# Kernel optimization log

Measured on AMD Instinct MI355X. Metric: run time of the kernel, lower is better.

## Reference

```python
import jax, jax.numpy as jnp
import numpy as np

E = 8        # num_experts
K = 2        # num_experts_per_tok
H = 1024     # hidden_dim
F = 2816     # intermediate_dim
R = 256      # shared-core rank
B, S = 2, 1024


def setup_inputs() -> dict:
    key = jax.random.key(0)
    ks = jax.random.split(key, 12)
    inp = {
        "hidden_states": jax.random.normal(ks[0], (B, S, H), jnp.float32),
        "gate_w": jax.random.normal(ks[1], (H, E), jnp.float32) / np.sqrt(H),
        # gate_proj: hidden -> intermediate, factored W_e = Ug[e] @ Cg @ Vg[e]
        "Ug": jax.random.normal(ks[2], (E, H, R), jnp.float32) / np.sqrt(H),
        "Cg": jax.random.normal(ks[3], (R, R), jnp.float32) / np.sqrt(R),
        "Vg": jax.random.normal(ks[4], (E, R, F), jnp.float32) / np.sqrt(R),
        # up_proj: hidden -> intermediate
        "Uu": jax.random.normal(ks[5], (E, H, R), jnp.float32) / np.sqrt(H),
        "Cu": jax.random.normal(ks[6], (R, R), jnp.float32) / np.sqrt(R),
        "Vu": jax.random.normal(ks[7], (E, R, F), jnp.float32) / np.sqrt(R),
        # down_proj: intermediate -> hidden
        "Ud": jax.random.normal(ks[8], (E, F, R), jnp.float32) / np.sqrt(F),
        "Cd": jax.random.normal(ks[9], (R, R), jnp.float32) / np.sqrt(R),
        "Vd": jax.random.normal(ks[10], (E, R, H), jnp.float32) / np.sqrt(R),
    }
    return inp


def _moe_forward(x, gate_w, Ug, Cg, Vg, Uu, Cu, Vu, Ud, Cd, Vd):
    b, s, h = x.shape
    xf = x.reshape(-1, h)                       # [T, H]
    T = xf.shape[0]
    logits = xf @ gate_w                        # [T, E]
    probs = jax.nn.softmax(logits, axis=-1)
    w, idx = jax.lax.top_k(probs, K)            # [T, K]
    w = w / jnp.sum(w, axis=-1, keepdims=True)
    # dense combine weights: combine[t, e] = sum of renormalized routing
    # weights over top-k slots routed to expert e (scatter-add in torch code)
    combine = jnp.zeros((T, E), xf.dtype).at[jnp.arange(T)[:, None], idx].add(w)
    out = jnp.zeros_like(xf)
    for e in range(E):  # fixed small expert count
        g = (xf @ Ug[e]) @ Cg @ Vg[e]           # [T, F]
        u = (xf @ Uu[e]) @ Cu @ Vu[e]           # [T, F]
        a = jax.nn.silu(g) * u
        y = (a @ Ud[e]) @ Cd @ Vd[e]            # [T, H]
        out = out + combine[:, e:e + 1] * y
    return out.reshape(b, s, h)


def reference(hidden_states, gate_w, Ug, Cg, Vg, Uu, Cu, Vu, Ud, Cd, Vd):
    return _moe_forward(hidden_states, gate_w, Ug, Cg, Vg, Uu, Cu, Vu, Ud, Cd, Vd)
```

## Files before the change

### kernel.cpp

```cpp
#include <hip/hip_runtime.h>
#include <math.h>

constexpr int cE = 8;
constexpr int cH = 1024;
constexpr int cF = 2816;
constexpr int cR = 256;
constexpr int cT = 2048;
constexpr int ROWS = cT * 2;
constexpr int LDA = 40;

using short8  = __attribute__((ext_vector_type(8))) short;
using float4v = __attribute__((ext_vector_type(4))) float;
#define MFMA16 __builtin_amdgcn_mfma_f32_16x16x32_bf16

__device__ __forceinline__ unsigned short f2bf(float f) {
  union { float f; unsigned u; } v; v.f = f;
  unsigned r = v.u + 0x7fffu + ((v.u >> 16) & 1u);
  return (unsigned short)(r >> 16);
}
__device__ __forceinline__ float bf2f(unsigned short s) {
  union { unsigned u; float f; } v; v.u = (unsigned)s << 16; return v.f;
}

__device__ __forceinline__ void store_bf8(unsigned short* dst, float4 a, float4 b) {
  union { unsigned short u[8]; uint4 v; } t;
  t.u[0] = f2bf(a.x); t.u[1] = f2bf(a.y); t.u[2] = f2bf(a.z); t.u[3] = f2bf(a.w);
  t.u[4] = f2bf(b.x); t.u[5] = f2bf(b.y); t.u[6] = f2bf(b.z); t.u[7] = f2bf(b.w);
  *reinterpret_cast<uint4*>(dst) = t.v;
}

__device__ __forceinline__ void gld16(const unsigned short* g, unsigned short* l) {
  __builtin_amdgcn_global_load_lds(
      (const __attribute__((address_space(1))) void*)g,
      (__attribute__((address_space(3))) void*)l, 16, 0, 0);
}

__device__ __forceinline__ void tconv_tile64(
    const float* __restrict__ in, unsigned short* __restrict__ out,
    int P, int Q, int e, int bx, int by, int tid, float (*tile)[65])
{
  const long es = (long)P * Q;
  in += e * es; out += e * es;
  const int c0 = bx * 64, r0 = by * 64;
  const int r = tid >> 4, c4 = (tid & 15) * 4;
#pragma unroll
  for (int p = 0; p < 4; ++p) {
    float4 v = *reinterpret_cast<const float4*>(
        in + (long)(r0 + p * 16 + r) * Q + c0 + c4);
    tile[p * 16 + r][c4 + 0] = v.x; tile[p * 16 + r][c4 + 1] = v.y;
    tile[p * 16 + r][c4 + 2] = v.z; tile[p * 16 + r][c4 + 3] = v.w;
  }
  __syncthreads();
  const int cc = tid >> 4, rr4 = (tid & 15) * 4;
#pragma unroll
  for (int p = 0; p < 4; ++p) {
    ushort4 o;
    o.x = f2bf(tile[rr4 + 0][p * 16 + cc]);
    o.y = f2bf(tile[rr4 + 1][p * 16 + cc]);
    o.z = f2bf(tile[rr4 + 2][p * 16 + cc]);
    o.w = f2bf(tile[rr4 + 3][p * 16 + cc]);
    *reinterpret_cast<ushort4*>(out + (long)(c0 + p * 16 + cc) * P + r0 + rr4) = o;
  }
}

constexpr int TCONV_BLOCKS = 4768;
constexpr int PREP1_BLOCKS = TCONV_BLOCKS + cT / 4;

__global__ __launch_bounds__(256) void k_prep1(
    const float* __restrict__ Cg, unsigned short* __restrict__ CgT,
    const float* __restrict__ Cu, unsigned short* __restrict__ CuT,
    const float* __restrict__ Vd, unsigned short* __restrict__ VdT,
    const float* __restrict__ Vg, unsigned short* __restrict__ vgT,
    const float* __restrict__ Vu, unsigned short* __restrict__ vuT,
    const float* __restrict__ Ud, unsigned short* __restrict__ udT,
    const float* __restrict__ x, const float* __restrict__ gw,
    unsigned short* __restrict__ xb, int* __restrict__ et,
    float* __restrict__ wt)
{
  __shared__ float tile[64][65];
  int b = blockIdx.x;
  const int tid = threadIdx.x;
  if (b < TCONV_BLOCKS) {
    const float* in; unsigned short* out; int P, Q;
    if (b < 16)         { in = Cg; out = CgT; P = 256;  Q = 256;  }
    else if (b < 32)    { b -= 16;    in = Cu; out = CuT; P = 256;  Q = 256;  }
    else if (b < 544)   { b -= 32;    in = Vd; out = VdT; P = 256;  Q = 1024; }
    else if (b < 1952)  { b -= 544;   in = Vg; out = vgT; P = 256;  Q = 2816; }
    else if (b < 3360)  { b -= 1952;  in = Vu; out = vuT; P = 256;  Q = 2816; }
    else                { b -= 3360;  in = Ud; out = udT; P = 2816; Q = 256;  }
    const int tpe = (P / 64) * (Q / 64);
    const int e = b / tpe, rem = b % tpe;
    const int bx = rem % (Q / 64), by = rem / (Q / 64);
    tconv_tile64(in, out, P, Q, e, bx, by, tid, tile);
    return;
  }
  const int wid = tid >> 6, lane = tid & 63;
  const int t = (b - TCONV_BLOCKS) * 4 + wid;
  const float* xr = x + (long)t * cH + lane * 16;
  float4 v0 = *reinterpret_cast<const float4*>(xr);
  float4 v1 = *reinterpret_cast<const float4*>(xr + 4);
  float4 v2 = *reinterpret_cast<const float4*>(xr + 8);
  float4 v3 = *reinterpret_cast<const float4*>(xr + 12);
  store_bf8(xb + (long)t * cH + lane * 16, v0, v1);
  store_bf8(xb + (long)t * cH + lane * 16 + 8, v2, v3);
  float xv[16];
  *reinterpret_cast<float4*>(&xv[0])  = v0;
  *reinterpret_cast<float4*>(&xv[4])  = v1;
  *reinterpret_cast<float4*>(&xv[8])  = v2;
  *reinterpret_cast<float4*>(&xv[12]) = v3;
  const float* g = gw + (long)lane * 16 * cE;
  float l[cE];
#pragma unroll
  for (int e = 0; e < cE; ++e) l[e] = 0.f;
#pragma unroll
  for (int i = 0; i < 16; ++i) {
    float4 ga = *reinterpret_cast<const float4*>(g + i * cE);
    float4 gb = *reinterpret_cast<const float4*>(g + i * cE + 4);
    float xi = xv[i];
    l[0] += xi * ga.x; l[1] += xi * ga.y; l[2] += xi * ga.z; l[3] += xi * ga.w;
    l[4] += xi * gb.x; l[5] += xi * gb.y; l[6] += xi * gb.z; l[7] += xi * gb.w;
  }
#pragma unroll
  for (int m = 1; m < 64; m <<= 1)
#pragma unroll
    for (int e = 0; e < cE; ++e)
      l[e] += __shfl_xor(l[e], m, 64);
  if (lane == 0) {
    int i0 = 0; float m0 = l[0];
#pragma unroll
    for (int e = 1; e < cE; ++e) if (l[e] > m0) { m0 = l[e]; i0 = e; }
    int i1 = -1; float m1 = -1e30f;
#pragma unroll
    for (int e = 0; e < cE; ++e) if (e != i0 && l[e] > m1) { m1 = l[e]; i1 = e; }
    float w0 = 1.f / (1.f + expf(m1 - m0));
    et[t * 2 + 0] = i0;  et[t * 2 + 1] = i1;
    wt[t * 2 + 0] = w0;  wt[t * 2 + 1] = 1.f - w0;
  }
}

__device__ __forceinline__ void foldm_body(
    const unsigned short* __restrict__ A, const float* __restrict__ B,
    unsigned short* __restrict__ D, int ldd, int m0, int n0, int tid,
    unsigned short* As, unsigned short* Bs)
{
  const int sr = tid >> 2, sk = (tid & 3) * 8;
  const unsigned short* a0 = A + (long)(m0 + sr) * 256 + sk;
  const unsigned short* a1 = a0 + (long)64 * 256;
  const float* br = B + (long)(n0 + sr) * 256 + sk;
  uint4 rA0, rA1; float4 rB0, rB1;
  auto load_slice = [&](int k0) {
    rA0 = *reinterpret_cast<const uint4*>(a0 + k0);
    rA1 = *reinterpret_cast<const uint4*>(a1 + k0);
    rB0 = *reinterpret_cast<const float4*>(br + k0);
    rB1 = *reinterpret_cast<const float4*>(br + k0 + 4);
  };
  load_slice(0);
  const int wid = tid >> 6, lane = tid & 63;
  const int wm = (wid >> 1) * 64, wn = (wid & 1) * 32;
  const int fr = lane & 15, fq = lane >> 4;
  float4v zf = {0.f, 0.f, 0.f, 0.f};
  float4v acc[4][2];
#pragma unroll
  for (int i = 0; i < 4; ++i) { acc[i][0] = zf; acc[i][1] = zf; }
  for (int k0 = 0; k0 < 256; k0 += 32) {
    *reinterpret_cast<uint4*>(&As[sr * LDA + sk]) = rA0;
    *reinterpret_cast<uint4*>(&As[(sr + 64) * LDA + sk]) = rA1;
    store_bf8(&Bs[sr * LDA + sk], rB0, rB1);
    if (k0 + 32 < 256) load_slice(k0 + 32);
    __syncthreads();
    short8 af[4], bf[2];
#pragma unroll
    for (int mi = 0; mi < 4; ++mi)
      af[mi] = *reinterpret_cast<const short8*>(&As[(wm + mi * 16 + fr) * LDA + fq * 8]);
#pragma unroll
    for (int nj = 0; nj < 2; ++nj)
      bf[nj] = *reinterpret_cast<const short8*>(&Bs[(wn + nj * 16 + fr) * LDA + fq * 8]);
#pragma unroll
    for (int mi = 0; mi < 4; ++mi)
#pragma unroll
      for (int nj = 0; nj < 2; ++nj)
        acc[mi][nj] = MFMA16(af[mi], bf[nj], acc[mi][nj], 0, 0, 0);
    __syncthreads();
  }
#pragma unroll
  for (int mi = 0; mi < 4; ++mi)
#pragma unroll
    for (int r = 0; r < 4; ++r) {
      int m = m0 + wm + mi * 16 + fq * 4 + r;
#pragma unroll
      for (int nj = 0; nj < 2; ++nj)
        D[(long)m * ldd + n0 + wn + nj * 16 + fr] = f2bf(acc[mi][nj][r]);
    }
}

constexpr int PREP2_BLOCKS = 512 + 256 + 1;
__global__ __launch_bounds__(256, 2) void k_prep2(
    const unsigned short* __restrict__ CgT, const unsigned short* __restrict__ CuT,
    const float* __restrict__ Ug, const float* __restrict__ Uu,
    unsigned short* __restrict__ b1t,
    const unsigned short* __restrict__ VdT, const float* __restrict__ Cd,
    unsigned short* __restrict__ vd2t,
    const int* __restrict__ et, int* __restrict__ rowmap,
    int* __restrict__ tok, int* __restrict__ cnt, int* __restrict__ off)
{
  __shared__ __align__(16) unsigned short As[128 * LDA], Bs[64 * LDA];
  __shared__ int sc_[cE], sp_[cE], so_[cE];
  const int b = blockIdx.x;
  const int tid = threadIdx.x;
  if (b < 512) {
    const int bx = b & 15, by = (b >> 4) & 1, z = b >> 5;
    const int sel = z >> 3, e = z & 7;
    const unsigned short* A = sel ? CuT : CgT;
    const float* B = (sel ? Uu : Ug) + (long)e * cH * cR;
    unsigned short* Dp = b1t + (long)e * 512 * 1024 + (long)sel * 256 * 1024;
    foldm_body(A, B, Dp, cH, by * 128, bx * 64, tid, As, Bs);
  } else if (b < 768) {
    const int b2 = b - 512;
    const int bx = b2 & 3, by = (b2 >> 2) & 7, e = b2 >> 5;
    foldm_body(VdT + (long)e * cH * cR, Cd, vd2t + (long)e * cH * 256, cR,
               by * 128, bx * 64, tid, As, Bs);
  } else {
    if (tid < cE) { sc_[tid] = 0; sp_[tid] = 0; }
    __syncthreads();
    for (int i = tid; i < ROWS; i += 256) atomicAdd(&sc_[et[i]], 1);
    __syncthreads();
    if (tid == 0) {
      int s = 0;
      for (int e = 0; e < cE; ++e) { so_[e] = s; s += sc_[e]; }
    }
    __syncthreads();
    for (int i = tid; i < ROWS; i += 256) {
      int e = et[i];
      int slot = atomicAdd(&sp_[e], 1);
      int cr = so_[e] + slot;
      rowmap[i] = cr;
      tok[cr] = i >> 1;
    }
    if (tid < cE) { cnt[tid] = sc_[tid]; off[tid] = so_[tid]; }
  }
}

__global__ __launch_bounds__(256, 3) void k_t1c(
    const unsigned short* __restrict__ xb, const unsigned short* __restrict__ b1t,
    unsigned short* __restrict__ t1, const int* __restrict__ tok,
    const int* __restrict__ cnt, const int* __restrict__ off)
{
  __shared__ __align__(16) unsigned short As[2][128 * 64], Bs[2][64 * 64];
  const int e = blockIdx.z, c = cnt[e], o = off[e];
  const int m0 = blockIdx.y * 128;
  if (m0 >= c) return;
  const int n0 = blockIdx.x * 64;
  const int tid = threadIdx.x;
  const int wid = tid >> 6, lane = tid & 63;
  const int sr8 = lane >> 3;
  const int scs = ((lane & 7) ^ sr8) * 8;
  const unsigned short* gA[4];
#pragma unroll
  for (int j = 0; j < 4; ++j) {
    int row = min(m0 + wid * 32 + j * 8 + sr8, c - 1);
    gA[j] = xb + (long)tok[o + row] * cH + scs;
  }
  const unsigned short* gB = b1t + (long)e * 512 * 1024 +
      (long)(n0 + wid * 16 + sr8) * 1024 + scs;
  const int lA = wid * 32 * 64;
  const int lB = wid * 16 * 64;
  auto STAGE = [&](int k0, int buf) {
#pragma unroll
    for (int j = 0; j < 4; ++j) gld16(gA[j] + k0, &As[buf][lA + j * 8 * 64]);
    gld16(gB + k0, &Bs[buf][lB]);
    gld16(gB + (long)8 * 1024 + k0, &Bs[buf][lB + 8 * 64]);
  };
  const int wm = (wid >> 1) * 64, wn = (wid & 1) * 32;
  const int fr = lane & 15, fq = lane >> 4;
  const int swz = (fr & 7) * 8;
  float4v zf = {0.f, 0.f, 0.f, 0.f};
  float4v acc[4][2];
#pragma unroll
  for (int i = 0; i < 4; ++i) { acc[i][0] = zf; acc[i][1] = zf; }
  STAGE(0, 0);
  __syncthreads();
  for (int t = 0; t < 16; ++t) {
    const int cur = t & 1;
    if (t < 15) STAGE((t + 1) * 64, cur ^ 1);
#pragma unroll
    for (int ks = 0; ks < 2; ++ks) {
      short8 af[4], bf[2];
#pragma unroll
      for (int mi = 0; mi < 4; ++mi)
        af[mi] = *reinterpret_cast<const short8*>(
            &As[cur][(wm + mi * 16 + fr) * 64 + ((ks * 32 + fq * 8) ^ swz)]);
#pragma unroll
      for (int nj = 0; nj < 2; ++nj)
        bf[nj] = *reinterpret_cast<const short8*>(
            &Bs[cur][(wn + nj * 16 + fr) * 64 + ((ks * 32 + fq * 8) ^ swz)]);
#pragma unroll
      for (int mi = 0; mi < 4; ++mi)
#pragma unroll
        for (int nj = 0; nj < 2; ++nj)
          acc[mi][nj] = MFMA16(af[mi], bf[nj], acc[mi][nj], 0, 0, 0);
    }
    __syncthreads();
  }
#pragma unroll
  for (int mi = 0; mi < 4; ++mi)
#pragma unroll
    for (int r = 0; r < 4; ++r) {
      int row = m0 + wm + mi * 16 + fq * 4 + r;
      if (row < c) {
#pragma unroll
        for (int nj = 0; nj < 2; ++nj)
          t1[(long)(o + row) * 512 + n0 + wn + nj * 16 + fr] = f2bf(acc[mi][nj][r]);
      }
    }
}

__global__ __launch_bounds__(256, 3) void k_act(
    const unsigned short* __restrict__ t1,
    const unsigned short* __restrict__ vgT, const unsigned short* __restrict__ vuT,
    unsigned short* __restrict__ a, const int* __restrict__ cnt,
    const int* __restrict__ off)
{
  __shared__ __align__(16) unsigned short Ag[2][128 * 32], Au[2][128 * 32];
  __shared__ __align__(16) unsigned short Bg[2][64 * 32],  Bu[2][64 * 32];
  const int e = blockIdx.z, c = cnt[e], o = off[e];
  const int m0 = blockIdx.y * 128;
  if (m0 >= c) return;
  const int n0 = blockIdx.x * 64;
  const int tid = threadIdx.x;
  const int wid = tid >> 6, lane = tid & 63;
  const int sr16 = lane >> 2;
  const int scs = (((lane & 3) ^ (sr16 & 3)) * 8);
  const int ra0 = o + min(m0 + wid * 32 + sr16, c - 1);
  const int ra1 = o + min(m0 + wid * 32 + 16 + sr16, c - 1);
  const unsigned short* gAg0 = t1 + (long)ra0 * 512 + scs;
  const unsigned short* gAg1 = t1 + (long)ra1 * 512 + scs;
  const unsigned short* gBg = vgT + (long)e * cF * 256 + (long)(n0 + wid * 16 + sr16) * 256 + scs;
  const unsigned short* gBu = vuT + (long)e * cF * 256 + (long)(n0 + wid * 16 + sr16) * 256 + scs;
  const int lA = wid * 32 * 32;
  const int lB = wid * 16 * 32;
  auto STAGE = [&](int k0, int buf) {
    gld16(gAg0 + k0, &Ag[buf][lA]);
    gld16(gAg1 + k0, &Ag[buf][lA + 16 * 32]);
    gld16(gAg0 + 256 + k0, &Au[buf][lA]);
    gld16(gAg1 + 256 + k0, &Au[buf][lA + 16 * 32]);
    gld16(gBg + k0, &Bg[buf][lB]);
    gld16(gBu + k0, &Bu[buf][lB]);
  };
  const int wm = (wid >> 1) * 64, wn = (wid & 1) * 32;
  const int fr = lane & 15, fq = lane >> 4;
  const int swz = (fr & 3) * 8;
  float4v zf = {0.f, 0.f, 0.f, 0.f};
  float4v accg[4][2], accu[4][2];
#pragma unroll
  for (int i = 0; i < 4; ++i) { accg[i][0] = zf; accg[i][1] = zf; accu[i][0] = zf; accu[i][1] = zf; }
  STAGE(0, 0);
  __syncthreads();
  for (int t = 0; t < 8; ++t) {
    const int cur = t & 1;
    if (t < 7) STAGE((t + 1) * 32, cur ^ 1);
    short8 ag[4], au[4], bg[2], bu[2];
#pragma unroll
    for (int mi = 0; mi < 4; ++mi) {
      ag[mi] = *reinterpret_cast<const short8*>(
          &Ag[cur][(wm + mi * 16 + fr) * 32 + ((fq * 8) ^ swz)]);
      au[mi] = *reinterpret_cast<const short8*>(
          &Au[cur][(wm + mi * 16 + fr) * 32 + ((fq * 8) ^ swz)]);
    }
#pragma unroll
    for (int nj = 0; nj < 2; ++nj) {
      bg[nj] = *reinterpret_cast<const short8*>(
          &Bg[cur][(wn + nj * 16 + fr) * 32 + ((fq * 8) ^ swz)]);
      bu[nj] = *reinterpret_cast<const short8*>(
          &Bu[cur][(wn + nj * 16 + fr) * 32 + ((fq * 8) ^ swz)]);
    }
#pragma unroll
    for (int mi = 0; mi < 4; ++mi)
#pragma unroll
      for (int nj = 0; nj < 2; ++nj) {
        accg[mi][nj] = MFMA16(ag[mi], bg[nj], accg[mi][nj], 0, 0, 0);
        accu[mi][nj] = MFMA16(au[mi], bu[nj], accu[mi][nj], 0, 0, 0);
      }
    __syncthreads();
  }
#pragma unroll
  for (int mi = 0; mi < 4; ++mi)
#pragma unroll
    for (int r = 0; r < 4; ++r) {
      int row = m0 + wm + mi * 16 + fq * 4 + r;
      if (row < c) {
#pragma unroll
        for (int nj = 0; nj < 2; ++nj) {
          float g = accg[mi][nj][r];
          float u = accu[mi][nj][r];
          float s = g / (1.f + expf(-g)) * u;
          a[(long)(o + row) * cF + n0 + wn + nj * 16 + fr] = f2bf(s);
        }
      }
    }
}

__global__ __launch_bounds__(256, 4) void k_t3(
    const unsigned short* __restrict__ a, const unsigned short* __restrict__ udT,
    float* __restrict__ t3p, const int* __restrict__ cnt,
    const int* __restrict__ off)
{
  __shared__ __align__(16) unsigned short As[2][64 * 64], Bs[2][64 * 64];
  const int e = blockIdx.z, c = cnt[e], o = off[e];
  const int m0 = blockIdx.y * 64;
  if (m0 >= c) return;
  const int n0 = (blockIdx.x & 3) * 64;
  const int ksp = blockIdx.x >> 2;
  const int kbase = ksp * 704;
  const int tid = threadIdx.x;
  const int wid = tid >> 6, lane = tid & 63;
  const int sr8 = lane >> 3;
  const int scs = ((lane & 7) ^ sr8) * 8;
  const int ra0 = o + min(m0 + wid * 16 + sr8, c - 1);
  const int ra1 = o + min(m0 + wid * 16 + 8 + sr8, c - 1);
  const unsigned short* gA0 = a + (long)ra0 * cF + kbase + scs;
  const unsigned short* gA1 = a + (long)ra1 * cF + kbase + scs;
  const unsigned short* gB  = udT + (long)e * 256 * cF +
      (long)(n0 + wid * 16 + sr8) * cF + kbase + scs;
  const int lofs = wid * 16 * 64;
  auto STAGE = [&](int k0, int buf) {
    gld16(gA0 + k0, &As[buf][lofs]);
    gld16(gA1 + k0, &As[buf][lofs + 8 * 64]);
    gld16(gB + k0, &Bs[buf][lofs]);
    gld16(gB + (long)8 * cF + k0, &Bs[buf][lofs + 8 * 64]);
  };
  const int wm = (wid >> 1) * 32, wn = (wid & 1) * 32;
  const int fr = lane & 15, fq = lane >> 4;
  const int swz = (fr & 7) * 8;
  float4v zf = {0.f, 0.f, 0.f, 0.f};
  float4v acc[2][2] = {{zf, zf}, {zf, zf}};
  STAGE(0, 0);
  __syncthreads();
  for (int t = 0; t < 11; ++t) {
    const int cur = t & 1;
    if (t < 10) STAGE((t + 1) * 64, cur ^ 1);
#pragma unroll
    for (int ks = 0; ks < 2; ++ks) {
      short8 af[2], bf[2];
#pragma unroll
      for (int mi = 0; mi < 2; ++mi)
        af[mi] = *reinterpret_cast<const short8*>(
            &As[cur][(wm + mi * 16 + fr) * 64 + ((ks * 32 + fq * 8) ^ swz)]);
#pragma unroll
      for (int nj = 0; nj < 2; ++nj)
        bf[nj] = *reinterpret_cast<const short8*>(
            &Bs[cur][(wn + nj * 16 + fr) * 64 + ((ks * 32 + fq * 8) ^ swz)]);
#pragma unroll
      for (int mi = 0; mi < 2; ++mi)
#pragma unroll
        for (int nj = 0; nj < 2; ++nj)
          acc[mi][nj] = MFMA16(af[mi], bf[nj], acc[mi][nj], 0, 0, 0);
    }
    __syncthreads();
  }
  float* dstbase = t3p + (long)ksp * ROWS * 256;
#pragma unroll
  for (int mi = 0; mi < 2; ++mi)
#pragma unroll
    for (int r = 0; r < 4; ++r) {
      int row = m0 + wm + mi * 16 + fq * 4 + r;
      if (row < c) {
        float* dst = dstbase + (long)(o + row) * 256 + n0 + wn;
#pragma unroll
        for (int nj = 0; nj < 2; ++nj)
          dst[nj * 16 + fr] = acc[mi][nj][r];
      }
    }
}

__global__ __launch_bounds__(256) void k_red(
    const float* __restrict__ t3p, unsigned short* __restrict__ t3b)
{
  const long psz = (long)ROWS * 256;
  long i = ((long)blockIdx.x * 256 + threadIdx.x) * 8;
  float4 s0 = *reinterpret_cast<const float4*>(t3p + i);
  float4 s1 = *reinterpret_cast<const float4*>(t3p + i + 4);
#pragma unroll
  for (int q = 1; q < 4; ++q) {
    float4 a0 = *reinterpret_cast<const float4*>(t3p + q * psz + i);
    float4 a1 = *reinterpret_cast<const float4*>(t3p + q * psz + i + 4);
    s0.x += a0.x; s0.y += a0.y; s0.z += a0.z; s0.w += a0.w;
    s1.x += a1.x; s1.y += a1.y; s1.z += a1.z; s1.w += a1.w;
  }
  store_bf8(t3b + i, s0, s1);
}

__global__ __launch_bounds__(256, 4) void k_y(
    const unsigned short* __restrict__ t3b, const unsigned short* __restrict__ vd2t,
    unsigned short* __restrict__ y, const int* __restrict__ cnt,
    const int* __restrict__ off)
{
  __shared__ __align__(16) unsigned short As[2][128 * 32], Bs[2][64 * 32];
  const int e = blockIdx.z, c = cnt[e], o = off[e];
  const int m0 = blockIdx.y * 128;
  if (m0 >= c) return;
  const int n0 = blockIdx.x * 64;
  const int tid = threadIdx.x;
  const int wid = tid >> 6, lane = tid & 63;
  const int sr16 = lane >> 2;
  const int scs = (((lane & 3) ^ (sr16 & 3)) * 8);
  const int ra0 = o + min(m0 + wid * 32 + sr16, c - 1);
  const int ra1 = o + min(m0 + wid * 32 + 16 + sr16, c - 1);
  const unsigned short* gA0 = t3b + (long)ra0 * 256 + scs;
  const unsigned short* gA1 = t3b + (long)ra1 * 256 + scs;
  const unsigned short* gB  = vd2t + (long)e * cH * 256 + (long)(n0 + wid * 16 + sr16) * 256 + scs;
  const int lA = wid * 32 * 32;
  const int lB = wid * 16 * 32;
  auto STAGE = [&](int k0, int buf) {
    gld16(gA0 + k0, &As[buf][lA]);
    gld16(gA1 + k0, &As[buf][lA + 16 * 32]);
    gld16(gB + k0, &Bs[buf][lB]);
  };
  const int wm = (wid >> 1) * 64, wn = (wid & 1) * 32;
  const int fr = lane & 15, fq = lane >> 4;
  const int swz = (fr & 3) * 8;
  float4v zf = {0.f, 0.f, 0.f, 0.f};
  float4v acc[4][2];
#pragma unroll
  for (int i = 0; i < 4; ++i) { acc[i][0] = zf; acc[i][1] = zf; }
  STAGE(0, 0);
  __syncthreads();
  for (int t = 0; t < 8; ++t) {
    const int cur = t & 1;
    if (t < 7) STAGE((t + 1) * 32, cur ^ 1);
    short8 af[4], bf[2];
#pragma unroll
    for (int mi = 0; mi < 4; ++mi)
      af[mi] = *reinterpret_cast<const short8*>(
          &As[cur][(wm + mi * 16 + fr) * 32 + ((fq * 8) ^ swz)]);
#pragma unroll
    for (int nj = 0; nj < 2; ++nj)
      bf[nj] = *reinterpret_cast<const short8*>(
          &Bs[cur][(wn + nj * 16 + fr) * 32 + ((fq * 8) ^ swz)]);
#pragma unroll
    for (int mi = 0; mi < 4; ++mi)
#pragma unroll
      for (int nj = 0; nj < 2; ++nj)
        acc[mi][nj] = MFMA16(af[mi], bf[nj], acc[mi][nj], 0, 0, 0);
    __syncthreads();
  }
#pragma unroll
  for (int mi = 0; mi < 4; ++mi)
#pragma unroll
    for (int r = 0; r < 4; ++r) {
      int row = m0 + wm + mi * 16 + fq * 4 + r;
      if (row < c) {
#pragma unroll
        for (int nj = 0; nj < 2; ++nj)
          y[(long)(o + row) * cH + n0 + wn + nj * 16 + fr] = f2bf(acc[mi][nj][r]);
      }
    }
}

__global__ __launch_bounds__(256) void k_combine(
    const unsigned short* __restrict__ y, const float* __restrict__ wt,
    const int* __restrict__ rowmap, float* __restrict__ out)
{
  const int tid = threadIdx.x;
  const int t = blockIdx.x * 2 + (tid >> 7);
  const int h = (tid & 127) * 8;
  const int r0 = rowmap[2 * t], r1 = rowmap[2 * t + 1];
  const float w0 = wt[2 * t], w1 = wt[2 * t + 1];
  union { uint4 v; unsigned short s[8]; } ua, ub;
  ua.v = *reinterpret_cast<const uint4*>(y + (long)r0 * cH + h);
  ub.v = *reinterpret_cast<const uint4*>(y + (long)r1 * cH + h);
  float o[8];
#pragma unroll
  for (int i = 0; i < 8; ++i)
    o[i] = w0 * bf2f(ua.s[i]) + w1 * bf2f(ub.s[i]);
  float* dst = out + (long)t * cH + h;
  *reinterpret_cast<float4*>(dst)     = make_float4(o[0], o[1], o[2], o[3]);
  *reinterpret_cast<float4*>(dst + 4) = make_float4(o[4], o[5], o[6], o[7]);
}

extern "C" void kernel_launch(void* const* d_in, const int* in_sizes, int n_in,
                              void* d_out, int out_size, void* d_ws, size_t ws_size,
                              hipStream_t stream)
{
  const float* x  = (const float*)d_in[0];
  const float* gw = (const float*)d_in[1];
  const float* Ug = (const float*)d_in[2];
  const float* Cg = (const float*)d_in[3];
  const float* Vg = (const float*)d_in[4];
  const float* Uu = (const float*)d_in[5];
  const float* Cu = (const float*)d_in[6];
  const float* Vu = (const float*)d_in[7];
  const float* Ud = (const float*)d_in[8];
  const float* Cd = (const float*)d_in[9];
  const float* Vd = (const float*)d_in[10];
  float* out = (float*)d_out;

  char* w = (char*)d_ws;
  unsigned short* vgT = (unsigned short*)w;
  float*          t3p = (float*)w;
  unsigned short* t3b = (unsigned short*)(w + (long)4 * ROWS * 256 * 4);
  w += (long)cE * cF * 256 * 2;
  unsigned short* b1t = (unsigned short*)w;  w += (long)cE * 512 * 1024 * 2;
  unsigned short* vd2t = (unsigned short*)w; w += (long)cE * cH * 256 * 2;
  unsigned short* vuT = (unsigned short*)w;
  unsigned short* yb  = (unsigned short*)w;  w += (long)cE * cF * 256 * 2;
  unsigned short* udT = (unsigned short*)w;  w += (long)cE * 256 * cF * 2;
  unsigned short* VdT = (unsigned short*)w;  w += (long)cE * cH * 256 * 2;
  unsigned short* xb  = (unsigned short*)w;  w += (long)cT * cH * 2;
  unsigned short* CgT = (unsigned short*)w;  w += (long)cR * cR * 2;
  unsigned short* CuT = (unsigned short*)w;  w += (long)cR * cR * 2;
  unsigned short* t1  = (unsigned short*)w;  w += (long)ROWS * 512 * 2;
  unsigned short* ab  = (unsigned short*)w;  w += (long)ROWS * cF * 2;
  float* wt   = (float*)w; w += ROWS * 4;
  int* et     = (int*)w; w += ROWS * 4;
  int* rowmap = (int*)w; w += ROWS * 4;
  int* tok    = (int*)w; w += ROWS * 4;
  int* cnt = (int*)w; w += cE * 4;
  int* off = (int*)w; w += cE * 4;

  k_prep1<<<dim3(PREP1_BLOCKS), dim3(256), 0, stream>>>(
      Cg, CgT, Cu, CuT, Vd, VdT, Vg, vgT, Vu, vuT, Ud, udT, x, gw, xb, et, wt);
  k_prep2<<<dim3(PREP2_BLOCKS), dim3(256), 0, stream>>>(
      CgT, CuT, Ug, Uu, b1t, VdT, Cd, vd2t, et, rowmap, tok, cnt, off);
  k_t1c<<<dim3(8, cT / 128, cE), dim3(256), 0, stream>>>(xb, b1t, t1, tok, cnt, off);
  k_act<<<dim3(cF / 64, cT / 128, cE), dim3(256), 0, stream>>>(t1, vgT, vuT, ab, cnt, off);
  k_t3<<<dim3(16, cT / 64, cE), dim3(256), 0, stream>>>(ab, udT, t3p, cnt, off);
  k_red<<<dim3(ROWS * 256 / (256 * 8)), dim3(256), 0, stream>>>(t3p, t3b);
  k_y<<<dim3(cH / 64, cT / 128, cE), dim3(256), 0, stream>>>(t3b, vd2t, yb, cnt, off);
  k_combine<<<dim3(cT / 2), dim3(256), 0, stream>>>(yb, wt, rowmap, out);
}
```

Before: 275.4 us.

## Move independent weight transposes from prep1 into prep2 to overlap with fold GEMMs

The large Vg/Vu/Ud transpose-convert tiles move out of the first prep kernel and into the second, where they run as extra blocks alongside the small fold GEMMs and the routing bookkeeping. Those GEMMs have too few blocks to fill the GPU, so the transposes can use the idle compute units instead of stretching the first kernel. Shared memory becomes one raw buffer reused by each branch, and launch bounds rise to three blocks per CU. This adds branch complexity, and occupancy limits on the GEMM blocks could change.

```diff
diff --git a/kernel.cpp b/kernel.cpp
--- a/kernel.cpp
+++ b/kernel.cpp
@@ -63,16 +63,13 @@
   }
 }
 
-constexpr int TCONV_BLOCKS = 4768;
-constexpr int PREP1_BLOCKS = TCONV_BLOCKS + cT / 4;
-
-__global__ __launch_bounds__(256) void k_prep1(
+constexpr int P1_TCONV = 544;
+constexpr int PREP1_BLOCKS = P1_TCONV + cT / 4;
+
+__global__ __launch_bounds__(256) void k_prep1s(
     const float* __restrict__ Cg, unsigned short* __restrict__ CgT,
     const float* __restrict__ Cu, unsigned short* __restrict__ CuT,
     const float* __restrict__ Vd, unsigned short* __restrict__ VdT,
-    const float* __restrict__ Vg, unsigned short* __restrict__ vgT,
-    const float* __restrict__ Vu, unsigned short* __restrict__ vuT,
-    const float* __restrict__ Ud, unsigned short* __restrict__ udT,
     const float* __restrict__ x, const float* __restrict__ gw,
     unsigned short* __restrict__ xb, int* __restrict__ et,
     float* __restrict__ wt)
@@ -80,14 +77,11 @@
   __shared__ float tile[64][65];
   int b = blockIdx.x;
   const int tid = threadIdx.x;
-  if (b < TCONV_BLOCKS) {
+  if (b < P1_TCONV) {
     const float* in; unsigned short* out; int P, Q;
-    if (b < 16)         { in = Cg; out = CgT; P = 256;  Q = 256;  }
-    else if (b < 32)    { b -= 16;    in = Cu; out = CuT; P = 256;  Q = 256;  }
-    else if (b < 544)   { b -= 32;    in = Vd; out = VdT; P = 256;  Q = 1024; }
-    else if (b < 1952)  { b -= 544;   in = Vg; out = vgT; P = 256;  Q = 2816; }
-    else if (b < 3360)  { b -= 1952;  in = Vu; out = vuT; P = 256;  Q = 2816; }
-    else                { b -= 3360;  in = Ud; out = udT; P = 2816; Q = 256;  }
+    if (b < 16)       { in = Cg; out = CgT; P = 256; Q = 256;  }
+    else if (b < 32)  { b -= 16; in = Cu; out = CuT; P = 256; Q = 256;  }
+    else              { b -= 32; in = Vd; out = VdT; P = 256; Q = 1024; }
     const int tpe = (P / 64) * (Q / 64);
     const int e = b / tpe, rem = b % tpe;
     const int bx = rem % (Q / 64), by = rem / (Q / 64);
@@ -95,7 +89,7 @@
     return;
   }
   const int wid = tid >> 6, lane = tid & 63;
-  const int t = (b - TCONV_BLOCKS) * 4 + wid;
+  const int t = (b - P1_TCONV) * 4 + wid;
   const float* xr = x + (long)t * cH + lane * 16;
   float4 v0 = *reinterpret_cast<const float4*>(xr);
   float4 v1 = *reinterpret_cast<const float4*>(xr + 4);
@@ -193,21 +187,25 @@
     }
 }
 
-constexpr int PREP2_BLOCKS = 512 + 256 + 1;
-__global__ __launch_bounds__(256, 2) void k_prep2(
+constexpr int PREP2_BLOCKS = 769 + 3 * 1408;
+__global__ __launch_bounds__(256, 3) void k_prep2(
     const unsigned short* __restrict__ CgT, const unsigned short* __restrict__ CuT,
     const float* __restrict__ Ug, const float* __restrict__ Uu,
     unsigned short* __restrict__ b1t,
     const unsigned short* __restrict__ VdT, const float* __restrict__ Cd,
     unsigned short* __restrict__ vd2t,
+    const float* __restrict__ Vg, unsigned short* __restrict__ vgT,
+    const float* __restrict__ Vu, unsigned short* __restrict__ vuT,
+    const float* __restrict__ Ud, unsigned short* __restrict__ udT,
     const int* __restrict__ et, int* __restrict__ rowmap,
     int* __restrict__ tok, int* __restrict__ cnt, int* __restrict__ off)
 {
-  __shared__ __align__(16) unsigned short As[128 * LDA], Bs[64 * LDA];
-  __shared__ int sc_[cE], sp_[cE], so_[cE];
+  __shared__ __align__(16) char smem[64 * 65 * 4];
   const int b = blockIdx.x;
   const int tid = threadIdx.x;
   if (b < 512) {
+    unsigned short* As = (unsigned short*)smem;
+    unsigned short* Bs = As + 128 * LDA;
     const int bx = b & 15, by = (b >> 4) & 1, z = b >> 5;
     const int sel = z >> 3, e = z & 7;
     const unsigned short* A = sel ? CuT : CgT;
@@ -215,11 +213,16 @@
     unsigned short* Dp = b1t + (long)e * 512 * 1024 + (long)sel * 256 * 1024;
     foldm_body(A, B, Dp, cH, by * 128, bx * 64, tid, As, Bs);
   } else if (b < 768) {
+    unsigned short* As = (unsigned short*)smem;
+    unsigned short* Bs = As + 128 * LDA;
     const int b2 = b - 512;
     const int bx = b2 & 3, by = (b2 >> 2) & 7, e = b2 >> 5;
     foldm_body(VdT + (long)e * cH * cR, Cd, vd2t + (long)e * cH * 256, cR,
                by * 128, bx * 64, tid, As, Bs);
-  } else {
+  } else if (b == 768) {
+    int* sc_ = (int*)smem;
+    int* sp_ = sc_ + cE;
+    int* so_ = sc_ + 2 * cE;
     if (tid < cE) { sc_[tid] = 0; sp_[tid] = 0; }
     __syncthreads();
     for (int i = tid; i < ROWS; i += 256) atomicAdd(&sc_[et[i]], 1);
@@ -237,6 +240,17 @@
       tok[cr] = i >> 1;
     }
     if (tid < cE) { cnt[tid] = sc_[tid]; off[tid] = so_[tid]; }
+  } else {
+    float (*tile)[65] = reinterpret_cast<float(*)[65]>(smem);
+    int t = b - 769;
+    const float* in; unsigned short* out; int P, Q;
+    if (t < 1408)       { in = Vg; out = vgT; P = 256;  Q = 2816; }
+    else if (t < 2816)  { t -= 1408; in = Vu; out = vuT; P = 256;  Q = 2816; }
+    else                { t -= 2816; in = Ud; out = udT; P = 2816; Q = 256;  }
+    const int tpe = (P / 64) * (Q / 64);
+    const int e = t / tpe, rem = t % tpe;
+    const int bx = rem % (Q / 64), by = rem / (Q / 64);
+    tconv_tile64(in, out, P, Q, e, bx, by, tid, tile);
   }
 }
 
@@ -617,10 +631,11 @@
   int* cnt = (int*)w; w += cE * 4;
   int* off = (int*)w; w += cE * 4;
 
-  k_prep1<<<dim3(PREP1_BLOCKS), dim3(256), 0, stream>>>(
-      Cg, CgT, Cu, CuT, Vd, VdT, Vg, vgT, Vu, vuT, Ud, udT, x, gw, xb, et, wt);
+  k_prep1s<<<dim3(PREP1_BLOCKS), dim3(256), 0, stream>>>(
+      Cg, CgT, Cu, CuT, Vd, VdT, x, gw, xb, et, wt);
   k_prep2<<<dim3(PREP2_BLOCKS), dim3(256), 0, stream>>>(
-      CgT, CuT, Ug, Uu, b1t, VdT, Cd, vd2t, et, rowmap, tok, cnt, off);
+      CgT, CuT, Ug, Uu, b1t, VdT, Cd, vd2t,
+      Vg, vgT, Vu, vuT, Ud, udT, et, rowmap, tok, cnt, off);
   k_t1c<<<dim3(8, cT / 128, cE), dim3(256), 0, stream>>>(xb, b1t, t1, tok, cnt, off);
   k_act<<<dim3(cF / 64, cT / 128, cE), dim3(256), 0, stream>>>(t1, vgT, vuT, ab, cnt, off);
   k_t3<<<dim3(16, cT / 64, cE), dim3(256), 0, stream>>>(ab, udT, t3p, cnt, off);
```

Result: faster. 264.8 us (-3.9%).
